# Kernel optimization log

Measured on AMD Instinct MI355X. Metric: run time of the kernel, lower is better.

Reference implementation:

```python
import jax, jax.numpy as jnp
import numpy as np

B, S, HID = 1, 2048, 2048
NH, NKV, HD = 16, 4, 128
G = NH // NKV  # queries per kv head (repeat_interleave factor)
QPA = 128      # query_pre_attn_scalar
EPS = 1e-6
SCALE = QPA ** -0.5
NEG = -1e9


def rms_norm(x, w, eps=EPS):
    return x * jax.lax.rsqrt(jnp.mean(x * x, axis=-1, keepdims=True) + eps) * w


def rope(x, cos, sin):
    # x: [B,S,H,D]; cos/sin: [S,D/2].
    # torch apply_rotary_emb: complex (x[:d/2] + i*x[d/2:]) * (cos + i*sin),
    # real parts -> first half, imag parts -> second half.
    d2 = x.shape[-1] // 2
    x1, x2 = x[..., :d2], x[..., d2:]
    c = cos[None, :, None, :]
    s = sin[None, :, None, :]
    return jnp.concatenate([x1 * c - x2 * s, x1 * s + x2 * c], axis=-1)


def setup_inputs() -> dict:
    key = jax.random.key(0)
    ks = jax.random.split(key, 4)
    hidden_states = jax.random.normal(ks[0], (B, S, HID), jnp.float32)
    inv_freq = 1.0 / (10000.0 ** (jnp.arange(0, HD, 2, dtype=jnp.float32) / HD))
    ang = jnp.arange(S, dtype=jnp.float32)[:, None] * inv_freq[None, :]  # [S, D/2]
    cos, sin = jnp.cos(ang), jnp.sin(ang)
    kv_write_indices = jnp.arange(S, dtype=jnp.int32)
    k_cache = jnp.zeros((B, S, NKV, HD), jnp.float32)
    v_cache = jnp.zeros((B, S, NKV, HD), jnp.float32)
    causal = jnp.tril(jnp.ones((S, S), dtype=bool))
    mask = jnp.where(causal, 0.0, NEG).astype(jnp.float32)[None, None]  # [1,1,S,S]
    qkv_out = (NH + 2 * NKV) * HD
    wqkv = jax.random.normal(ks[1], (qkv_out, HID), jnp.float32) * 0.02
    bqkv = jnp.zeros((qkv_out,), jnp.float32)
    wo = jax.random.normal(ks[2], (HID, NH * HD), jnp.float32) * 0.02
    bo = jnp.zeros((HID,), jnp.float32)
    q_norm_w = jnp.ones((HD,), jnp.float32)
    k_norm_w = jnp.ones((HD,), jnp.float32)
    return {"hidden_states": hidden_states, "cos": cos, "sin": sin,
            "k_cache": k_cache, "v_cache": v_cache, "mask": mask,
            "wqkv": wqkv, "bqkv": bqkv, "wo": wo, "bo": bo,
            "q_norm_w": q_norm_w, "k_norm_w": k_norm_w,
            "kv_write_indices": kv_write_indices}


def reference(hidden_states, cos, sin, k_cache, v_cache, mask,
              wqkv, bqkv, wo, bo, q_norm_w, k_norm_w, kv_write_indices):
    qkv = hidden_states @ wqkv.T + bqkv  # [B,S,(NH+2*NKV)*HD]
    q_sz, kv_sz = NH * HD, NKV * HD
    xq = qkv[..., :q_sz].reshape(B, S, NH, HD)
    xk = qkv[..., q_sz:q_sz + kv_sz].reshape(B, S, NKV, HD)
    xv = qkv[..., q_sz + kv_sz:].reshape(B, S, NKV, HD)
    xq = rope(rms_norm(xq, q_norm_w), cos, sin)
    xk = rope(rms_norm(xk, k_norm_w), cos, sin)
    k = k_cache.at[:, kv_write_indices].set(xk)  # index_copy_ on dim 1
    v = v_cache.at[:, kv_write_indices].set(xv)
    # GQA: head h attends with kv head h // G (repeat_interleave order)
    q = (xq * SCALE).reshape(B, S, NKV, G, HD)
    scores = jnp.einsum('bskgd,btkd->bkgst', q, k) + mask[:, :, None]  # [B,NKV,G,S,T]
    p = jax.nn.softmax(scores.astype(jnp.float32), axis=-1).astype(q.dtype)
    out = jnp.einsum('bkgst,btkd->bskgd', p, v).reshape(B, S, NH * HD)
    return out @ wo.T + bo
```

## Files before the change

### kernel.cpp

```cpp
#include <hip/hip_runtime.h>
#include <stdint.h>

#define S_LEN 2048
#define HIDN  2048
#define NH    16
#define NKV   4
#define HD    128
#define QKV_N 3072
#define Q_SZ  2048
#define SCALE_Q 0.088388347648318447f

typedef __attribute__((ext_vector_type(8))) short  short8;
typedef __attribute__((ext_vector_type(4))) float  f32x4;

__device__ __forceinline__ uint16_t f2bf(float f) {
  uint32_t u = __float_as_uint(f);
  u += 0x7fffu + ((u >> 16) & 1u);
  return (uint16_t)(u >> 16);
}

__device__ __forceinline__ void gload16(const void* g, void* lds_wave_base) {
  __builtin_amdgcn_global_load_lds(
      (const __attribute__((address_space(1))) uint32_t*)(uintptr_t)g,
      (__attribute__((address_space(3))) uint32_t*)(uint32_t)(uintptr_t)lds_wave_base,
      16, 0, 0);
}

__global__ __launch_bounds__(256) void cvt3_kernel(const float* __restrict__ a, uint16_t* __restrict__ oa, int na,
                                                   const float* __restrict__ b, uint16_t* __restrict__ ob, int nb,
                                                   const float* __restrict__ c, uint16_t* __restrict__ oc, int nc) {
  int i = (blockIdx.x * 256 + threadIdx.x) * 4;
  const float* src; uint16_t* dst; int j;
  if (i < na)           { src = a; dst = oa; j = i; }
  else if (i < na + nb) { src = b; dst = ob; j = i - na; }
  else if (i < na + nb + nc) { src = c; dst = oc; j = i - na - nb; }
  else return;
  float4 v = *(const float4*)(src + j);
  ushort4 o;
  o.x = f2bf(v.x); o.y = f2bf(v.y); o.z = f2bf(v.z); o.w = f2bf(v.w);
  *(ushort4*)(dst + j) = o;
}

#define BM 128
#define BN 128
#define BK 64
__global__ __launch_bounds__(512) void gemm_nt(const uint16_t* __restrict__ A,
                                               const uint16_t* __restrict__ B,
                                               const float* __restrict__ bias,
                                               float* __restrict__ C,
                                               int M, int N, int K) {
  __shared__ uint16_t As[2][BM * BK];
  __shared__ uint16_t Bs[2][BN * BK];
  const int tid = threadIdx.x;
  const int m0 = blockIdx.y * BM;
  const int n0 = blockIdx.x * BN;
  const int lane = tid & 63;
  const int w = tid >> 6;
  const int wm = (w >> 2) * 64, wn = (w & 3) * 32;
  const int lr = lane & 15, lg = lane >> 4;
  const int wb = w << 10;
  const int lb = wb + lane * 16;

  f32x4 acc[4][2];
#pragma unroll
  for (int i = 0; i < 4; ++i)
#pragma unroll
    for (int j = 0; j < 2; ++j) acc[i][j] = (f32x4){0.f, 0.f, 0.f, 0.f};

  auto stage = [&](int buf, int k0) {
#pragma unroll
    for (int i = 0; i < 2; ++i) {
      int bofs = i * 8192 + lb;
      int row = bofs >> 7;
      int colb = (bofs & 127) ^ ((row & 7) << 4);
      gload16((const char*)A + ((size_t)(m0 + row) * K + k0) * 2 + colb,
              (char*)As[buf] + i * 8192 + wb);
      gload16((const char*)B + ((size_t)(n0 + row) * K + k0) * 2 + colb,
              (char*)Bs[buf] + i * 8192 + wb);
    }
  };

  stage(0, 0);
  __syncthreads();
  const int nk = K / BK;
  for (int kk = 0; kk < nk; ++kk) {
    const int cur = kk & 1;
    if (kk + 1 < nk) stage(cur ^ 1, (kk + 1) * BK);
#pragma unroll
    for (int ks = 0; ks < 2; ++ks) {
      short8 av[4], bv[2];
#pragma unroll
      for (int i = 0; i < 4; ++i) {
        int row = wm + i * 16 + lr;
        av[i] = *(const short8*)((const char*)As[cur] + row * 128 + ((ks * 64 + lg * 16) ^ ((lr & 7) << 4)));
      }
#pragma unroll
      for (int j = 0; j < 2; ++j) {
        int row = wn + j * 16 + lr;
        bv[j] = *(const short8*)((const char*)Bs[cur] + row * 128 + ((ks * 64 + lg * 16) ^ ((lr & 7) << 4)));
      }
#pragma unroll
      for (int i = 0; i < 4; ++i)
#pragma unroll
        for (int j = 0; j < 2; ++j)
          acc[i][j] = __builtin_amdgcn_mfma_f32_16x16x32_bf16(av[i], bv[j], acc[i][j], 0, 0, 0);
    }
    __syncthreads();
  }
#pragma unroll
  for (int i = 0; i < 4; ++i) {
#pragma unroll
    for (int j = 0; j < 2; ++j) {
      int col = n0 + wn + j * 16 + lr;
      float bb = bias ? bias[col] : 0.f;
#pragma unroll
      for (int r = 0; r < 4; ++r) {
        int rowg = m0 + wm + i * 16 + lg * 4 + r;
        C[(size_t)rowg * N + col] = acc[i][j][r] + bb;
      }
    }
  }
}

#define QK_BLK (S_LEN * 20 / 4)
#define VT_BLK (NKV * (S_LEN / 64) * (HD / 64))
__global__ __launch_bounds__(256) void post_kernel(const float* __restrict__ qkv,
                                                   const float* __restrict__ cosb,
                                                   const float* __restrict__ sinb,
                                                   const float* __restrict__ qw,
                                                   const float* __restrict__ kw,
                                                   const int* __restrict__ widx,
                                                   uint16_t* __restrict__ Qo,
                                                   uint16_t* __restrict__ Ko,
                                                   uint16_t* __restrict__ Vt) {
  __shared__ float tile[64][68];
  int tid = threadIdx.x;
  if (blockIdx.x < QK_BLK) {
    int row = blockIdx.x * 4 + (tid >> 6);
    int lane = tid & 63;
    int t = row / 20, head = row % 20;
    bool isq = head < NH;
    int off = isq ? head * HD : Q_SZ + (head - NH) * HD;
    const float* x = qkv + (size_t)t * QKV_N + off;
    float x1 = x[lane], x2 = x[lane + 64];
    float ss = x1 * x1 + x2 * x2;
#pragma unroll
    for (int m = 1; m < 64; m <<= 1) ss += __shfl_xor(ss, m, 64);
    float rs = rsqrtf(ss * (1.0f / 128.0f) + 1e-6f);
    const float* wn_ = isq ? qw : kw;
    float n1 = x1 * rs * wn_[lane], n2 = x2 * rs * wn_[lane + 64];
    float c = cosb[t * 64 + lane], s = sinb[t * 64 + lane];
    float o1 = n1 * c - n2 * s;
    float o2 = n1 * s + n2 * c;
    if (isq) {
      o1 *= SCALE_Q; o2 *= SCALE_Q;
      uint16_t* dst = Qo + ((size_t)head * S_LEN + t) * HD;
      dst[lane] = f2bf(o1); dst[lane + 64] = f2bf(o2);
    } else {
      int td = widx[t];
      uint16_t* dst = Ko + ((size_t)(head - NH) * S_LEN + td) * HD;
      dst[lane] = f2bf(o1); dst[lane + 64] = f2bf(o2);
    }
  } else {
    int b = blockIdx.x - QK_BLK;
    int dt = b & 1;
    int tt = (b >> 1) & 31;
    int kh = b >> 6;
    int r = tid >> 2, c0 = tid & 3;
    const float* src = qkv + (size_t)(tt * 64 + r) * QKV_N + Q_SZ + NKV * HD + kh * HD + dt * 64;
#pragma unroll
    for (int i = 0; i < 4; ++i) {
      float4 v = *(const float4*)(src + (c0 + i * 4) * 4);
      *(float4*)&tile[r][(c0 + i * 4) * 4] = v;
    }
    __syncthreads();
    int rd = tid >> 2;
#pragma unroll
    for (int j = 0; j < 16; ++j) {
      int tloc = c0 * 16 + j;
      int tg = widx[tt * 64 + tloc];
      Vt[(size_t)(kh * HD + dt * 64 + rd) * S_LEN + tg] = f2bf(tile[tloc][rd]);
    }
  }
}

__global__ __launch_bounds__(256) void attn_kernel(const uint16_t* __restrict__ Q,
                                                   const uint16_t* __restrict__ Kc,
                                                   const uint16_t* __restrict__ Vt,
                                                   uint16_t* __restrict__ O) {
  __shared__ uint16_t Ks[2][64 * 128];
  __shared__ uint16_t Vs[2][128 * 64];
  __shared__ uint16_t Ps[4][16 * 64];

  const int x = blockIdx.x;
  const int half = x >> 8, rem = x & 255;
  const int h = rem >> 4, slot = rem & 15;
  const int qt = half ? slot : 31 - slot;
  const int kh = h >> 2;
  const int tid = threadIdx.x, w = tid >> 6, lane = tid & 63;
  const int lr = lane & 15, lg = lane >> 4;
  const int wb = w << 10, lb = wb + lane * 16;

  auto stage = [&](int buf, int t0) {
#pragma unroll
    for (int i = 0; i < 4; ++i) {
      int b = i * 4096 + lb;
      int rowK = b >> 8, colK = b & 255;
      gload16((const char*)Kc + ((size_t)kh * S_LEN + t0 + rowK) * (HD * 2) + (colK ^ ((rowK & 7) << 4)),
              (char*)Ks[buf] + i * 4096 + wb);
      int rowV = b >> 7, colV = b & 127;
      gload16((const char*)Vt + ((size_t)(kh * HD + rowV) * S_LEN + t0) * 2 + (colV ^ ((rowV & 7) << 4)),
              (char*)Vs[buf] + i * 4096 + wb);
    }
  };

  const int q0 = qt * 64;
  const int qw0 = q0 + w * 16;
  const int qg = qw0 + lr;

  short8 qf[4];
  const uint16_t* qb = Q + ((size_t)h * S_LEN + qw0 + lr) * HD;
#pragma unroll
  for (int ks = 0; ks < 4; ++ks) qf[ks] = *(const short8*)(qb + ks * 32 + lg * 8);

  f32x4 o[8];
#pragma unroll
  for (int d = 0; d < 8; ++d) o[d] = (f32x4){0.f, 0.f, 0.f, 0.f};
  float mrun = -1e30f, lrun = 0.f;

  const int ntiles = qt + 1;
  stage(0, 0);
  __syncthreads();

  for (int tt = 0; tt < ntiles; ++tt) {
    const int cur = tt & 1;
    const int t0 = tt * 64;
    if (tt + 1 < ntiles) stage(cur ^ 1, t0 + 64);

    f32x4 st[4];
    __builtin_amdgcn_s_setprio(1);
#pragma unroll
    for (int ts = 0; ts < 4; ++ts) {
      st[ts] = (f32x4){0.f, 0.f, 0.f, 0.f};
#pragma unroll
      for (int ks = 0; ks < 4; ++ks) {
        int row = ts * 16 + lr;
        int cb = (ks * 64 + lg * 16) ^ ((row & 7) << 4);
        short8 kf = *(const short8*)((const char*)Ks[cur] + row * 256 + cb);
        st[ts] = __builtin_amdgcn_mfma_f32_16x16x32_bf16(kf, qf[ks], st[ts], 0, 0, 0);
      }
    }
    __builtin_amdgcn_s_setprio(0);

    float pvv[4][4];
    float pm = -1e30f;
    if (tt == ntiles - 1) {
#pragma unroll
      for (int ts = 0; ts < 4; ++ts)
#pragma unroll
        for (int r = 0; r < 4; ++r) {
          int tglob = t0 + ts * 16 + lg * 4 + r;
          float sv = (tglob > qg) ? -1e9f : st[ts][r];
          pvv[ts][r] = sv;
          pm = fmaxf(pm, sv);
        }
    } else {
#pragma unroll
      for (int ts = 0; ts < 4; ++ts)
#pragma unroll
        for (int r = 0; r < 4; ++r) {
          pvv[ts][r] = st[ts][r];
          pm = fmaxf(pm, st[ts][r]);
        }
    }
    pm = fmaxf(pm, __shfl_xor(pm, 16, 64));
    pm = fmaxf(pm, __shfl_xor(pm, 32, 64));
    float mnew = fmaxf(mrun, pm);
    float scl = __expf(mrun - mnew);
    float psum = 0.f;
#pragma unroll
    for (int ts = 0; ts < 4; ++ts)
#pragma unroll
      for (int r = 0; r < 4; ++r) {
        pvv[ts][r] = __expf(pvv[ts][r] - mnew);
        psum += pvv[ts][r];
      }
    psum += __shfl_xor(psum, 16, 64);
    psum += __shfl_xor(psum, 32, 64);
    lrun = lrun * scl + psum;
    mrun = mnew;

    {
      uint32_t* pw = (uint32_t*)&Ps[w][0];
#pragma unroll
      for (int ts = 0; ts < 4; ++ts)
#pragma unroll
        for (int rr = 0; rr < 2; ++rr) {
          uint32_t pp = (uint32_t)f2bf(pvv[ts][2 * rr]) | ((uint32_t)f2bf(pvv[ts][2 * rr + 1]) << 16);
          pw[lr * 32 + ((ts * 8 + lg * 2 + rr) ^ ((lr & 7) << 2))] = pp;
        }
    }

#pragma unroll
    for (int r = 0; r < 4; ++r) {
      float s4 = __shfl(scl, (lane & 48) | (lg * 4 + r), 64);
#pragma unroll
      for (int d = 0; d < 8; ++d) o[d][r] *= s4;
    }

    __builtin_amdgcn_s_setprio(1);
#pragma unroll
    for (int ks = 0; ks < 2; ++ks) {
      short8 pf = *(const short8*)((const char*)&Ps[w][0] + lr * 128 + ((ks * 64 + lg * 16) ^ ((lr & 7) << 4)));
#pragma unroll
      for (int d = 0; d < 8; ++d) {
        int row = d * 16 + lr;
        int cb = (ks * 64 + lg * 16) ^ ((row & 7) << 4);
        short8 vf = *(const short8*)((const char*)Vs[cur] + row * 128 + cb);
        o[d] = __builtin_amdgcn_mfma_f32_16x16x32_bf16(pf, vf, o[d], 0, 0, 0);
      }
    }
    __builtin_amdgcn_s_setprio(0);

    __syncthreads();
  }

#pragma unroll
  for (int r = 0; r < 4; ++r) {
    float ls = __shfl(lrun, (lane & 48) | (lg * 4 + r), 64);
    float inv = 1.0f / ls;
    int qg2 = qw0 + lg * 4 + r;
    uint16_t* dst = O + ((size_t)qg2 * NH + h) * HD;
#pragma unroll
    for (int d = 0; d < 8; ++d) dst[d * 16 + lr] = f2bf(o[d][r] * inv);
  }
}

extern "C" void kernel_launch(void* const* d_in, const int* in_sizes, int n_in,
                              void* d_out, int out_size, void* d_ws, size_t ws_size,
                              hipStream_t stream) {
  const float* hidden = (const float*)d_in[0];
  const float* cosb   = (const float*)d_in[1];
  const float* sinb   = (const float*)d_in[2];
  const float* wqkv = (const float*)d_in[6];
  const float* bqkv = (const float*)d_in[7];
  const float* wo   = (const float*)d_in[8];
  const float* bo   = (const float*)d_in[9];
  const float* qnw  = (const float*)d_in[10];
  const float* knw  = (const float*)d_in[11];
  const int*   widx = (const int*)d_in[12];
  float* out = (float*)d_out;

  char* ws = (char*)d_ws;
  uint16_t* hb    = (uint16_t*)(ws);
  uint16_t* wqb   = (uint16_t*)(ws + (8u  << 20));
  uint16_t* wob   = (uint16_t*)(ws + (20u << 20));
  float*    qkv   = (float*)   (ws + (28u << 20));
  uint16_t* Qb    = (uint16_t*)(ws + (52u << 20));
  uint16_t* Kb    = (uint16_t*)(ws + (60u << 20));
  uint16_t* Vtb   = (uint16_t*)(ws + (62u << 20));
  uint16_t* attnb = (uint16_t*)(ws);

  const int na = S_LEN * HIDN, nb = QKV_N * HIDN, nc = HIDN * HIDN;
  cvt3_kernel<<<(na + nb + nc) / 4 / 256, 256, 0, stream>>>(hidden, hb, na, wqkv, wqb, nb, wo, wob, nc);

  gemm_nt<<<dim3(QKV_N / BN, S_LEN / BM), 512, 0, stream>>>(hb, wqb, bqkv, qkv,
                                                            S_LEN, QKV_N, HIDN);
  post_kernel<<<QK_BLK + VT_BLK, 256, 0, stream>>>(qkv, cosb, sinb, qnw, knw, widx, Qb, Kb, Vtb);
  attn_kernel<<<512, 256, 0, stream>>>(Qb, Kb, Vtb, attnb);
  gemm_nt<<<dim3(HIDN / BN, S_LEN / BM), 512, 0, stream>>>(attnb, wob, bo, out,
                                                           S_LEN, HIDN, HIDN);
}
```

Baseline: 255.5 us.

## Use exp2 softmax with lazy rescaling and hardware packed bf16 conversion

Folds log2(e) into the query scale so the softmax uses exp2f directly. Adds a lazy online-softmax rescale: when no row's tile max exceeds the running max by more than 8, the running max is kept and the per-tile rescale of the output accumulators is skipped. Replaces software round-to-nearest bf16 packing with the v_cvt_pk_bf16_f32 instruction in both the P store and the input conversion kernel. This trims VALU and exp work in the attention inner loop, at the cost of a wave-wide vote per tile and P values that can grow up to 2^8 before being stored in bf16.

```diff
diff --git a/kernel.cpp b/kernel.cpp
--- a/kernel.cpp
+++ b/kernel.cpp
@@ -8,7 +8,7 @@
 #define HD    128
 #define QKV_N 3072
 #define Q_SZ  2048
-#define SCALE_Q 0.088388347648318447f
+#define SCALE_Q 0.12751743f
 
 typedef __attribute__((ext_vector_type(8))) short  short8;
 typedef __attribute__((ext_vector_type(4))) float  f32x4;
@@ -17,6 +17,12 @@
   uint32_t u = __float_as_uint(f);
   u += 0x7fffu + ((u >> 16) & 1u);
   return (uint16_t)(u >> 16);
+}
+
+__device__ __forceinline__ uint32_t cvtpk(float lo, float hi) {
+  uint32_t r;
+  asm("v_cvt_pk_bf16_f32 %0, %1, %2" : "=v"(r) : "v"(lo), "v"(hi));
+  return r;
 }
 
 __device__ __forceinline__ void gload16(const void* g, void* lds_wave_base) {
@@ -36,9 +42,10 @@
   else if (i < na + nb + nc) { src = c; dst = oc; j = i - na - nb; }
   else return;
   float4 v = *(const float4*)(src + j);
-  ushort4 o;
-  o.x = f2bf(v.x); o.y = f2bf(v.y); o.z = f2bf(v.z); o.w = f2bf(v.w);
-  *(ushort4*)(dst + j) = o;
+  uint2 o;
+  o.x = cvtpk(v.x, v.y);
+  o.y = cvtpk(v.z, v.w);
+  *(uint2*)(dst + j) = o;
 }
 
 #define BM 128
@@ -252,60 +259,59 @@
     }
     __builtin_amdgcn_s_setprio(0);
 
-    float pvv[4][4];
-    float pm = -1e30f;
     if (tt == ntiles - 1) {
 #pragma unroll
       for (int ts = 0; ts < 4; ++ts)
 #pragma unroll
         for (int r = 0; r < 4; ++r) {
           int tglob = t0 + ts * 16 + lg * 4 + r;
-          float sv = (tglob > qg) ? -1e9f : st[ts][r];
-          pvv[ts][r] = sv;
-          pm = fmaxf(pm, sv);
+          if (tglob > qg) st[ts][r] = -1e9f;
         }
-    } else {
-#pragma unroll
-      for (int ts = 0; ts < 4; ++ts)
-#pragma unroll
-        for (int r = 0; r < 4; ++r) {
-          pvv[ts][r] = st[ts][r];
-          pm = fmaxf(pm, st[ts][r]);
-        }
-    }
+    }
+
+    float pm = -1e30f;
+#pragma unroll
+    for (int ts = 0; ts < 4; ++ts)
+#pragma unroll
+      for (int r = 0; r < 4; ++r) pm = fmaxf(pm, st[ts][r]);
     pm = fmaxf(pm, __shfl_xor(pm, 16, 64));
     pm = fmaxf(pm, __shfl_xor(pm, 32, 64));
-    float mnew = fmaxf(mrun, pm);
-    float scl = __expf(mrun - mnew);
+
+    const bool defer = __all(pm <= mrun + 8.0f) != 0;
+    const float mnew = defer ? mrun : fmaxf(mrun, pm);
+
     float psum = 0.f;
 #pragma unroll
     for (int ts = 0; ts < 4; ++ts)
 #pragma unroll
       for (int r = 0; r < 4; ++r) {
-        pvv[ts][r] = __expf(pvv[ts][r] - mnew);
-        psum += pvv[ts][r];
+        st[ts][r] = exp2f(st[ts][r] - mnew);
+        psum += st[ts][r];
       }
     psum += __shfl_xor(psum, 16, 64);
     psum += __shfl_xor(psum, 32, 64);
-    lrun = lrun * scl + psum;
-    mrun = mnew;
+
+    if (!defer) {
+      float scl = exp2f(mrun - mnew);
+      lrun *= scl;
+      mrun = mnew;
+#pragma unroll
+      for (int r = 0; r < 4; ++r) {
+        float s4 = __shfl(scl, (lane & 48) | (lg * 4 + r), 64);
+#pragma unroll
+        for (int d = 0; d < 8; ++d) o[d][r] *= s4;
+      }
+    }
+    lrun += psum;
 
     {
       uint32_t* pw = (uint32_t*)&Ps[w][0];
 #pragma unroll
       for (int ts = 0; ts < 4; ++ts)
 #pragma unroll
-        for (int rr = 0; rr < 2; ++rr) {
-          uint32_t pp = (uint32_t)f2bf(pvv[ts][2 * rr]) | ((uint32_t)f2bf(pvv[ts][2 * rr + 1]) << 16);
-          pw[lr * 32 + ((ts * 8 + lg * 2 + rr) ^ ((lr & 7) << 2))] = pp;
-        }
-    }
-
-#pragma unroll
-    for (int r = 0; r < 4; ++r) {
-      float s4 = __shfl(scl, (lane & 48) | (lg * 4 + r), 64);
-#pragma unroll
-      for (int d = 0; d < 8; ++d) o[d][r] *= s4;
+        for (int rr = 0; rr < 2; ++rr)
+          pw[lr * 32 + ((ts * 8 + lg * 2 + rr) ^ ((lr & 7) << 2))] =
+              cvtpk(st[ts][2 * rr], st[ts][2 * rr + 1]);
     }
 
     __builtin_amdgcn_s_setprio(1);
```

Measured after the change: 255.2 us. No clear change (-0.1%).
